# Performance work log

Hardware: AMD Instinct MI355X
Metric: run time of the kernel (lower is better)

The kernel has to match this reference:

```python
import jax, jax.numpy as jnp
import numpy as np

N_HEADS, EMB_DIM, K_DIM, V_DIM = 16, 1024, 64, 64
B, L = 4, 2048


def setup_inputs() -> dict:
    key = jax.random.key(0)
    ks = jax.random.split(key, 7)
    scale = 1.0 / np.sqrt(EMB_DIM)
    return {
        "query": jax.random.normal(ks[0], (B, L, EMB_DIM), dtype=jnp.float32),
        "key": jax.random.normal(ks[1], (B, L, EMB_DIM), dtype=jnp.float32),
        "value": jax.random.normal(ks[2], (B, L, EMB_DIM), dtype=jnp.float32),
        "pad_mask": jnp.ones((B, L), dtype=jnp.int32),
        # Linear weights stored as (in, out); torch Linear computes x @ W.T with W (out, in)
        "Wq": jax.random.normal(ks[3], (EMB_DIM, N_HEADS * K_DIM), dtype=jnp.float32) * scale,
        "Wk": jax.random.normal(ks[4], (EMB_DIM, N_HEADS * K_DIM), dtype=jnp.float32) * scale,
        "Wv": jax.random.normal(ks[5], (EMB_DIM, N_HEADS * V_DIM), dtype=jnp.float32) * scale,
        "Wo": jax.random.normal(ks[6], (N_HEADS * V_DIM, EMB_DIM), dtype=jnp.float32) * scale,
    }


def reference(query, key, value, pad_mask, Wq, Wk, Wv, Wo):
    batch, Lq, _ = query.shape
    Lk = key.shape[1]
    # projections -> [B, L, H, dk/dv]
    q = (query @ Wq).reshape(batch, Lq, N_HEADS, K_DIM)
    k = (key @ Wk).reshape(batch, Lk, N_HEADS, K_DIM)
    v = (value @ Wv).reshape(batch, Lk, N_HEADS, V_DIM)
    # logits: [B, H, Lq, Lk], scaled by 1/sqrt(dk)
    logits = jnp.einsum("bqhd,bkhd->bhqk", q, k) / np.sqrt(K_DIM).astype(np.float32)
    # causal mask: disallow j > i
    causal = jnp.tril(jnp.ones((Lq, Lk), dtype=bool))
    logits = jnp.where(causal[None, None], logits, -jnp.inf)
    # pad mask: positions with pad_mask == 0 are masked out
    keep = (pad_mask != 0)[:, None, None, :]  # [B,1,1,Lk]
    logits = jnp.where(keep, logits, -jnp.inf)
    probs = jax.nn.softmax(logits, axis=-1)
    attn = jnp.einsum("bhqk,bkhd->bqhd", probs, v).reshape(batch, Lq, N_HEADS * V_DIM)
    return attn @ Wo
```

## Files before the change

### kernel.cpp

```cpp
#include <hip/hip_runtime.h>
#include <hip/hip_bf16.h>

typedef short bf16x8 __attribute__((ext_vector_type(8)));
typedef float f32x4 __attribute__((ext_vector_type(4)));

#define EMB 1024
#define NH 16
#define SEQ 2048
#define BATCH 4
#define MROWS (BATCH * SEQ)

static __device__ inline unsigned short f2bf(float f) {
  unsigned u = __float_as_uint(f);
  u += 0x7fffu + ((u >> 16) & 1u);
  return (unsigned short)(u >> 16);
}

static __device__ inline unsigned cvtpk(float lo, float hi) {
  unsigned r;
  asm("v_cvt_pk_bf16_f32 %0, %1, %2" : "=v"(r) : "v"(lo), "v"(hi));
  return r;
}

static __device__ inline void gload16(const void* g, void* l) {
  __builtin_amdgcn_global_load_lds(
      (const __attribute__((address_space(1))) unsigned int*)g,
      (__attribute__((address_space(3))) unsigned int*)l, 16, 0, 0);
}

__global__ __launch_bounds__(256) void wtrans_kernel(
    const float* w0, const float* w1, const float* w2, const float* w3,
    unsigned short* o0, unsigned short* o1, unsigned short* o2, unsigned short* o3) {
  __shared__ float t[32][33];
  int z = blockIdx.z;
  const float* W = z == 0 ? w0 : z == 1 ? w1 : z == 2 ? w2 : w3;
  unsigned short* O = z == 0 ? o0 : z == 1 ? o1 : z == 2 ? o2 : o3;
  float sc = (z == 0) ? 0.18033688011112042f : 1.0f;
  int bx = blockIdx.x * 32;
  int by = blockIdx.y * 32;
  int tx = threadIdx.x, ty = threadIdx.y;
#pragma unroll
  for (int j = 0; j < 4; ++j)
    t[ty + j * 8][tx] = W[(size_t)(bx + ty + j * 8) * EMB + by + tx];
  __syncthreads();
#pragma unroll
  for (int j = 0; j < 4; ++j)
    O[(size_t)(by + ty + j * 8) * EMB + bx + tx] = f2bf(t[tx][ty + j * 8] * sc);
}

template <int IN_F32, int OUT_MODE>
__global__ __launch_bounds__(256) void gemm_kernel(const void* Ap, const unsigned short* Bt, void* Cp) {
  __shared__ __align__(16) unsigned short As[128 * 64];
  __shared__ __align__(16) unsigned short Bs[128 * 64];
  const int K = EMB;
  int tid = threadIdx.x;
  int lane = tid & 63, wave = tid >> 6;
  int q = lane & 15, g = lane >> 4;
  int qx7 = q & 7;
  int wm = (wave >> 1) * 64, wn = (wave & 1) * 64;
  int lin = blockIdx.x + (blockIdx.y << 3);
  int idx = (lin & 7) * 64 + (lin >> 3);
  int tm = (idx >> 3) * 128, tn = (idx & 7) * 128;
  f32x4 acc[4][4] = {};
  for (int kt = 0; kt < K; kt += 64) {
    if (IN_F32) {
      const float* A = (const float*)Ap;
#pragma unroll
      for (int it = 0; it < 4; ++it) {
        int gid = tid + it * 256;
        int row = gid >> 3, cb = gid & 7;
        const float4* s0 = (const float4*)(A + (size_t)(tm + row) * K + kt + cb * 8);
        float4 x = s0[0], y = s0[1];
        uint4 w;
        w.x = cvtpk(x.x, x.y); w.y = cvtpk(x.z, x.w);
        w.z = cvtpk(y.x, y.y); w.w = cvtpk(y.z, y.w);
        *(uint4*)&As[row * 64 + 8 * (cb ^ (row & 7))] = w;
      }
    } else {
      const unsigned short* A = (const unsigned short*)Ap;
#pragma unroll
      for (int it = 0; it < 4; ++it) {
        int gid = tid + it * 256;
        int row = gid >> 3, cb = gid & 7;
        gload16(A + (size_t)(tm + row) * K + kt + 8 * (cb ^ (row & 7)), &As[gid * 8]);
      }
    }
#pragma unroll
    for (int it = 0; it < 4; ++it) {
      int gid = tid + it * 256;
      int row = gid >> 3, cb = gid & 7;
      gload16(Bt + (size_t)(tn + row) * K + kt + 8 * (cb ^ (row & 7)), &Bs[gid * 8]);
    }
    __syncthreads();
#pragma unroll
    for (int s = 0; s < 2; ++s) {
      bf16x8 af[4], bfr[4];
#pragma unroll
      for (int mf = 0; mf < 4; ++mf)
        af[mf] = *(const bf16x8*)&As[(wm + mf * 16 + q) * 64 + 8 * ((4 * s + g) ^ qx7)];
#pragma unroll
      for (int nf = 0; nf < 4; ++nf)
        bfr[nf] = *(const bf16x8*)&Bs[(wn + nf * 16 + q) * 64 + 8 * ((4 * s + g) ^ qx7)];
#pragma unroll
      for (int mf = 0; mf < 4; ++mf)
#pragma unroll
        for (int nf = 0; nf < 4; ++nf)
          acc[mf][nf] = __builtin_amdgcn_mfma_f32_16x16x32_bf16(af[mf], bfr[nf], acc[mf][nf], 0, 0, 0);
    }
    __syncthreads();
  }
  if (OUT_MODE == 0) {
    unsigned short* C = (unsigned short*)Cp;
#pragma unroll
    for (int mf = 0; mf < 4; ++mf)
#pragma unroll
      for (int nf = 0; nf < 4; ++nf)
#pragma unroll
        for (int r = 0; r < 4; ++r) {
          int row = tm + wm + mf * 16 + 4 * g + r;
          int col = tn + wn + nf * 16 + q;
          C[(size_t)row * EMB + col] = f2bf(acc[mf][nf][r]);
        }
  } else if (OUT_MODE == 1) {
    unsigned short* C = (unsigned short*)Cp;
#pragma unroll
    for (int mf = 0; mf < 4; ++mf) {
      int m0 = tm + wm + mf * 16 + 4 * g;
      int b = m0 >> 11, l = m0 & 2047;
#pragma unroll
      for (int nf = 0; nf < 4; ++nf) {
        int n = tn + wn + nf * 16 + q;
        int h = n >> 6, dv = n & 63;
        uint2 w;
        w.x = cvtpk(acc[mf][nf][0], acc[mf][nf][1]);
        w.y = cvtpk(acc[mf][nf][2], acc[mf][nf][3]);
        *(uint2*)&C[(((size_t)b * NH + h) * 64 + dv) * SEQ + l] = w;
      }
    }
  } else {
    float* C = (float*)Cp;
#pragma unroll
    for (int mf = 0; mf < 4; ++mf)
#pragma unroll
      for (int nf = 0; nf < 4; ++nf)
#pragma unroll
        for (int r = 0; r < 4; ++r) {
          int row = tm + wm + mf * 16 + 4 * g + r;
          int col = tn + wn + nf * 16 + q;
          C[(size_t)row * EMB + col] = acc[mf][nf][r];
        }
  }
}

__global__ __launch_bounds__(256) void attn_kernel(
    const unsigned short* Qb, const unsigned short* Kb, const unsigned short* VTb,
    const int* pad, unsigned short* Ob) {
  __shared__ __align__(16) unsigned short Ks[2][64 * 64];
  __shared__ __align__(16) unsigned short Vs[2][64 * 64];
  __shared__ __align__(16) unsigned short Ps[4][16 * 64];
  int tid = threadIdx.x;
  int lane = tid & 63, wave = tid >> 6;
  int q = lane & 15, g = lane >> 4;
  int qx7 = q & 7;
  int lin = blockIdx.x;
  int idx = (lin & 7) * 128 + (lin >> 3);
  int b = idx >> 8, h = (idx >> 4) & 15, px = idx & 15;

  int srow = tid >> 3, scb = tid & 7;
  int ssw = 8 * (scb ^ (srow & 7));
  const unsigned short* Kbase = Kb + (size_t)b * SEQ * EMB + (size_t)srow * EMB + h * 64 + ssw;
  const unsigned short* Vbase = VTb + (((size_t)(b * NH + h)) * 64 + srow) * SEQ + ssw;

#pragma unroll 1
  for (int half = 0; half < 2; ++half) {
    int c = half ? 31 - px : px;
    int qg = c * 64 + wave * 16 + q;
    const unsigned short* Qrow = Qb + ((size_t)(b * SEQ + qg)) * EMB + h * 64;
    bf16x8 qf0 = *(const bf16x8*)(Qrow + 8 * g);
    bf16x8 qf1 = *(const bf16x8*)(Qrow + 32 + 8 * g);
    f32x4 o[4] = {};
    float m_run = -INFINITY, l_run = 0.f;

#pragma unroll
    for (int it = 0; it < 2; ++it) {
      gload16(Kbase + (size_t)(it * 32) * EMB, &Ks[0][(tid + it * 256) * 8]);
      gload16(Vbase + it * 32 * SEQ, &Vs[0][(tid + it * 256) * 8]);
    }
    __syncthreads();

#pragma unroll 1
    for (int t = 0; t <= c; ++t) {
      int kvt = t * 64;
      int cur = t & 1;
      if (t < c) {
#pragma unroll
        for (int it = 0; it < 2; ++it) {
          gload16(Kbase + (size_t)(kvt + 64 + it * 32) * EMB, &Ks[cur ^ 1][(tid + it * 256) * 8]);
          gload16(Vbase + (size_t)(kvt + 64) + it * 32 * SEQ, &Vs[cur ^ 1][(tid + it * 256) * 8]);
        }
      }
      int pv = pad[b * SEQ + kvt + lane];
      unsigned long long pmask = __ballot(pv != 0);
      f32x4 sf[4] = {};
      __builtin_amdgcn_s_setprio(1);
#pragma unroll
      for (int s = 0; s < 2; ++s) {
#pragma unroll
        for (int mf = 0; mf < 4; ++mf) {
          bf16x8 kf = *(const bf16x8*)&Ks[cur][(mf * 16 + q) * 64 + 8 * ((4 * s + g) ^ qx7)];
          sf[mf] = __builtin_amdgcn_mfma_f32_16x16x32_bf16(kf, s ? qf1 : qf0, sf[mf], 0, 0, 0);
        }
      }
      __builtin_amdgcn_s_setprio(0);
      float tmax = -INFINITY;
      bool full = (t < c) && (pmask == ~0ull);
      if (full) {
#pragma unroll
        for (int mf = 0; mf < 4; ++mf)
#pragma unroll
          for (int r = 0; r < 4; ++r) tmax = fmaxf(tmax, sf[mf][r]);
      } else {
#pragma unroll
        for (int mf = 0; mf < 4; ++mf)
#pragma unroll
          for (int r = 0; r < 4; ++r) {
            int kvl = mf * 16 + 4 * g + r;
            bool keep = (kvt + kvl <= qg) && ((pmask >> kvl) & 1ULL);
            float sv = keep ? sf[mf][r] : -INFINITY;
            sf[mf][r] = sv;
            tmax = fmaxf(tmax, sv);
          }
      }
      tmax = fmaxf(tmax, __shfl_xor(tmax, 16));
      tmax = fmaxf(tmax, __shfl_xor(tmax, 32));
      if (!__all(tmax <= m_run + 8.0f)) {
        float m_new = fmaxf(m_run, tmax);
        float alpha = __builtin_amdgcn_exp2f(m_run - m_new);
        l_run *= alpha;
#pragma unroll
        for (int mv = 0; mv < 4; ++mv) o[mv] *= alpha;
        m_run = m_new;
      }
      float rsum = 0.f;
      float pvv[16];
#pragma unroll
      for (int mf = 0; mf < 4; ++mf)
#pragma unroll
        for (int r = 0; r < 4; ++r) {
          float p = __builtin_amdgcn_exp2f(sf[mf][r] - m_run);
          pvv[mf * 4 + r] = p;
          rsum += p;
        }
#pragma unroll
      for (int mf = 0; mf < 4; ++mf) {
        uint2 w;
        w.x = cvtpk(pvv[mf * 4 + 0], pvv[mf * 4 + 1]);
        w.y = cvtpk(pvv[mf * 4 + 2], pvv[mf * 4 + 3]);
        int cbP = 2 * mf + (g >> 1);
        *(uint2*)&Ps[wave][q * 64 + 8 * (cbP ^ qx7) + 4 * (g & 1)] = w;
      }
      rsum += __shfl_xor(rsum, 16);
      rsum += __shfl_xor(rsum, 32);
      l_run += rsum;
      __builtin_amdgcn_s_setprio(1);
#pragma unroll
      for (int s = 0; s < 2; ++s) {
        bf16x8 pb = *(const bf16x8*)&Ps[wave][q * 64 + 8 * ((4 * s + g) ^ qx7)];
#pragma unroll
        for (int mv = 0; mv < 4; ++mv) {
          bf16x8 va = *(const bf16x8*)&Vs[cur][(mv * 16 + q) * 64 + 8 * ((4 * s + g) ^ qx7)];
          o[mv] = __builtin_amdgcn_mfma_f32_16x16x32_bf16(va, pb, o[mv], 0, 0, 0);
        }
      }
      __builtin_amdgcn_s_setprio(0);
      __syncthreads();
    }
    float inv = 1.0f / l_run;
    unsigned short* Orow = Ob + ((size_t)(b * SEQ + qg)) * EMB + h * 64;
#pragma unroll
    for (int mv = 0; mv < 4; ++mv) {
      uint2 w;
      w.x = cvtpk(o[mv][0] * inv, o[mv][1] * inv);
      w.y = cvtpk(o[mv][2] * inv, o[mv][3] * inv);
      *(uint2*)&Orow[mv * 16 + 4 * g] = w;
    }
  }
}

extern "C" void kernel_launch(void* const* d_in, const int* in_sizes, int n_in,
                              void* d_out, int out_size, void* d_ws, size_t ws_size,
                              hipStream_t stream) {
  const float* query = (const float*)d_in[0];
  const float* key   = (const float*)d_in[1];
  const float* value = (const float*)d_in[2];
  const int*   pad   = (const int*)d_in[3];
  const float* Wq = (const float*)d_in[4];
  const float* Wk = (const float*)d_in[5];
  const float* Wv = (const float*)d_in[6];
  const float* Wo = (const float*)d_in[7];

  unsigned short* WqT = (unsigned short*)d_ws;
  unsigned short* WkT = WqT + (size_t)EMB * EMB;
  unsigned short* WvT = WkT + (size_t)EMB * EMB;
  unsigned short* WoT = WvT + (size_t)EMB * EMB;
  unsigned short* Qb  = WoT + (size_t)EMB * EMB;
  unsigned short* Kb  = Qb + (size_t)MROWS * EMB;
  unsigned short* VTb = Kb + (size_t)MROWS * EMB;
  unsigned short* Ab  = VTb + (size_t)MROWS * EMB;

  wtrans_kernel<<<dim3(EMB / 32, EMB / 32, 4), dim3(32, 8), 0, stream>>>(
      Wq, Wk, Wv, Wo, WqT, WkT, WvT, WoT);
  gemm_kernel<1, 0><<<dim3(8, 64), 256, 0, stream>>>(query, WqT, Qb);
  gemm_kernel<1, 0><<<dim3(8, 64), 256, 0, stream>>>(key, WkT, Kb);
  gemm_kernel<1, 1><<<dim3(8, 64), 256, 0, stream>>>(value, WvT, VTb);
  attn_kernel<<<dim3(1024), 256, 0, stream>>>(Qb, Kb, VTb, pad, Ab);
  gemm_kernel<0, 2><<<dim3(8, 64), 256, 0, stream>>>(Ab, WoT, d_out);
}
```

Before: 208.4 us.

## Process both causal query tiles in one KV pass to share K/V loads

The attention kernel used to handle its two paired query tiles (px and 31-px) one after the other, streaming K/V twice. Now both tiles' state is kept in registers and a single KV sweep up to the longer tile's length serves both. The shorter tile's work is predicated off once its causal limit is passed. This removes redundant K/V global/LDS loads and gives each wave more independent MFMA work per tile, at the cost of extra registers and LDS for a second P buffer, which may reduce occupancy.

```diff
diff --git a/kernel.cpp b/kernel.cpp
--- a/kernel.cpp
+++ b/kernel.cpp
@@ -157,7 +157,8 @@
     const int* pad, unsigned short* Ob) {
   __shared__ __align__(16) unsigned short Ks[2][64 * 64];
   __shared__ __align__(16) unsigned short Vs[2][64 * 64];
-  __shared__ __align__(16) unsigned short Ps[4][16 * 64];
+  __shared__ __align__(16) unsigned short PsA[4][16 * 64];
+  __shared__ __align__(16) unsigned short PsB[4][16 * 64];
   int tid = threadIdx.x;
   int lane = tid & 63, wave = tid >> 6;
   int q = lane & 15, g = lane >> 4;
@@ -165,125 +166,195 @@
   int lin = blockIdx.x;
   int idx = (lin & 7) * 128 + (lin >> 3);
   int b = idx >> 8, h = (idx >> 4) & 15, px = idx & 15;
+  int cA = px, cB = 31 - px;
+  int qgA = cA * 64 + wave * 16 + q;
+  int qgB = cB * 64 + wave * 16 + q;
+
+  const unsigned short* QrowA = Qb + ((size_t)(b * SEQ + qgA)) * EMB + h * 64;
+  const unsigned short* QrowB = Qb + ((size_t)(b * SEQ + qgB)) * EMB + h * 64;
+  bf16x8 qfA0 = *(const bf16x8*)(QrowA + 8 * g);
+  bf16x8 qfA1 = *(const bf16x8*)(QrowA + 32 + 8 * g);
+  bf16x8 qfB0 = *(const bf16x8*)(QrowB + 8 * g);
+  bf16x8 qfB1 = *(const bf16x8*)(QrowB + 32 + 8 * g);
+
+  f32x4 oA[4] = {}, oB[4] = {};
+  float mA = -INFINITY, lA = 0.f, mB = -INFINITY, lB = 0.f;
 
   int srow = tid >> 3, scb = tid & 7;
   int ssw = 8 * (scb ^ (srow & 7));
   const unsigned short* Kbase = Kb + (size_t)b * SEQ * EMB + (size_t)srow * EMB + h * 64 + ssw;
   const unsigned short* Vbase = VTb + (((size_t)(b * NH + h)) * 64 + srow) * SEQ + ssw;
 
+#pragma unroll
+  for (int it = 0; it < 2; ++it) {
+    gload16(Kbase + (size_t)(it * 32) * EMB, &Ks[0][(tid + it * 256) * 8]);
+    gload16(Vbase + (size_t)(it * 32) * SEQ, &Vs[0][(tid + it * 256) * 8]);
+  }
+  __syncthreads();
+
 #pragma unroll 1
-  for (int half = 0; half < 2; ++half) {
-    int c = half ? 31 - px : px;
-    int qg = c * 64 + wave * 16 + q;
-    const unsigned short* Qrow = Qb + ((size_t)(b * SEQ + qg)) * EMB + h * 64;
-    bf16x8 qf0 = *(const bf16x8*)(Qrow + 8 * g);
-    bf16x8 qf1 = *(const bf16x8*)(Qrow + 32 + 8 * g);
-    f32x4 o[4] = {};
-    float m_run = -INFINITY, l_run = 0.f;
-
-#pragma unroll
-    for (int it = 0; it < 2; ++it) {
-      gload16(Kbase + (size_t)(it * 32) * EMB, &Ks[0][(tid + it * 256) * 8]);
-      gload16(Vbase + it * 32 * SEQ, &Vs[0][(tid + it * 256) * 8]);
-    }
-    __syncthreads();
-
-#pragma unroll 1
-    for (int t = 0; t <= c; ++t) {
-      int kvt = t * 64;
-      int cur = t & 1;
-      if (t < c) {
-#pragma unroll
-        for (int it = 0; it < 2; ++it) {
-          gload16(Kbase + (size_t)(kvt + 64 + it * 32) * EMB, &Ks[cur ^ 1][(tid + it * 256) * 8]);
-          gload16(Vbase + (size_t)(kvt + 64) + it * 32 * SEQ, &Vs[cur ^ 1][(tid + it * 256) * 8]);
-        }
-      }
-      int pv = pad[b * SEQ + kvt + lane];
-      unsigned long long pmask = __ballot(pv != 0);
-      f32x4 sf[4] = {};
-      __builtin_amdgcn_s_setprio(1);
-#pragma unroll
-      for (int s = 0; s < 2; ++s) {
-#pragma unroll
-        for (int mf = 0; mf < 4; ++mf) {
-          bf16x8 kf = *(const bf16x8*)&Ks[cur][(mf * 16 + q) * 64 + 8 * ((4 * s + g) ^ qx7)];
-          sf[mf] = __builtin_amdgcn_mfma_f32_16x16x32_bf16(kf, s ? qf1 : qf0, sf[mf], 0, 0, 0);
-        }
-      }
-      __builtin_amdgcn_s_setprio(0);
+  for (int t = 0; t <= cB; ++t) {
+    int kvt = t * 64;
+    int cur = t & 1;
+    if (t < cB) {
+#pragma unroll
+      for (int it = 0; it < 2; ++it) {
+        gload16(Kbase + (size_t)(kvt + 64 + it * 32) * EMB, &Ks[cur ^ 1][(tid + it * 256) * 8]);
+        gload16(Vbase + (size_t)(kvt + 64) + (size_t)(it * 32) * SEQ, &Vs[cur ^ 1][(tid + it * 256) * 8]);
+      }
+    }
+    int pv = pad[b * SEQ + kvt + lane];
+    unsigned long long pmask = __ballot(pv != 0);
+    bool doA = (t <= cA);
+
+    f32x4 sfA[4] = {}, sfB[4] = {};
+    __builtin_amdgcn_s_setprio(1);
+#pragma unroll
+    for (int s = 0; s < 2; ++s) {
+#pragma unroll
+      for (int mf = 0; mf < 4; ++mf) {
+        bf16x8 kf = *(const bf16x8*)&Ks[cur][(mf * 16 + q) * 64 + 8 * ((4 * s + g) ^ qx7)];
+        if (doA) sfA[mf] = __builtin_amdgcn_mfma_f32_16x16x32_bf16(kf, s ? qfA1 : qfA0, sfA[mf], 0, 0, 0);
+        sfB[mf] = __builtin_amdgcn_mfma_f32_16x16x32_bf16(kf, s ? qfB1 : qfB0, sfB[mf], 0, 0, 0);
+      }
+    }
+    __builtin_amdgcn_s_setprio(0);
+
+    if (doA) {
       float tmax = -INFINITY;
-      bool full = (t < c) && (pmask == ~0ull);
+      bool full = (t < cA) && (pmask == ~0ull);
       if (full) {
 #pragma unroll
         for (int mf = 0; mf < 4; ++mf)
 #pragma unroll
-          for (int r = 0; r < 4; ++r) tmax = fmaxf(tmax, sf[mf][r]);
+          for (int r = 0; r < 4; ++r) tmax = fmaxf(tmax, sfA[mf][r]);
       } else {
 #pragma unroll
         for (int mf = 0; mf < 4; ++mf)
 #pragma unroll
           for (int r = 0; r < 4; ++r) {
             int kvl = mf * 16 + 4 * g + r;
-            bool keep = (kvt + kvl <= qg) && ((pmask >> kvl) & 1ULL);
-            float sv = keep ? sf[mf][r] : -INFINITY;
-            sf[mf][r] = sv;
+            bool keep = (kvt + kvl <= qgA) && ((pmask >> kvl) & 1ULL);
+            float sv = keep ? sfA[mf][r] : -INFINITY;
+            sfA[mf][r] = sv;
             tmax = fmaxf(tmax, sv);
           }
       }
       tmax = fmaxf(tmax, __shfl_xor(tmax, 16));
       tmax = fmaxf(tmax, __shfl_xor(tmax, 32));
-      if (!__all(tmax <= m_run + 8.0f)) {
-        float m_new = fmaxf(m_run, tmax);
-        float alpha = __builtin_amdgcn_exp2f(m_run - m_new);
-        l_run *= alpha;
-#pragma unroll
-        for (int mv = 0; mv < 4; ++mv) o[mv] *= alpha;
-        m_run = m_new;
+      if (!__all(tmax <= mA + 8.0f)) {
+        float m_new = fmaxf(mA, tmax);
+        float alpha = __builtin_amdgcn_exp2f(mA - m_new);
+        lA *= alpha;
+#pragma unroll
+        for (int mv = 0; mv < 4; ++mv) oA[mv] *= alpha;
+        mA = m_new;
       }
       float rsum = 0.f;
-      float pvv[16];
+      float pv0[16];
 #pragma unroll
       for (int mf = 0; mf < 4; ++mf)
 #pragma unroll
         for (int r = 0; r < 4; ++r) {
-          float p = __builtin_amdgcn_exp2f(sf[mf][r] - m_run);
-          pvv[mf * 4 + r] = p;
+          float p = __builtin_amdgcn_exp2f(sfA[mf][r] - mA);
+          pv0[mf * 4 + r] = p;
           rsum += p;
         }
 #pragma unroll
       for (int mf = 0; mf < 4; ++mf) {
         uint2 w;
-        w.x = cvtpk(pvv[mf * 4 + 0], pvv[mf * 4 + 1]);
-        w.y = cvtpk(pvv[mf * 4 + 2], pvv[mf * 4 + 3]);
+        w.x = cvtpk(pv0[mf * 4 + 0], pv0[mf * 4 + 1]);
+        w.y = cvtpk(pv0[mf * 4 + 2], pv0[mf * 4 + 3]);
         int cbP = 2 * mf + (g >> 1);
-        *(uint2*)&Ps[wave][q * 64 + 8 * (cbP ^ qx7) + 4 * (g & 1)] = w;
+        *(uint2*)&PsA[wave][q * 64 + 8 * (cbP ^ qx7) + 4 * (g & 1)] = w;
       }
       rsum += __shfl_xor(rsum, 16);
       rsum += __shfl_xor(rsum, 32);
-      l_run += rsum;
-      __builtin_amdgcn_s_setprio(1);
-#pragma unroll
-      for (int s = 0; s < 2; ++s) {
-        bf16x8 pb = *(const bf16x8*)&Ps[wave][q * 64 + 8 * ((4 * s + g) ^ qx7)];
-#pragma unroll
-        for (int mv = 0; mv < 4; ++mv) {
-          bf16x8 va = *(const bf16x8*)&Vs[cur][(mv * 16 + q) * 64 + 8 * ((4 * s + g) ^ qx7)];
-          o[mv] = __builtin_amdgcn_mfma_f32_16x16x32_bf16(va, pb, o[mv], 0, 0, 0);
+      lA += rsum;
+    }
+
+    {
+      float tmax = -INFINITY;
+      bool full = (t < cB) && (pmask == ~0ull);
+      if (full) {
+#pragma unroll
+        for (int mf = 0; mf < 4; ++mf)
+#pragma unroll
+          for (int r = 0; r < 4; ++r) tmax = fmaxf(tmax, sfB[mf][r]);
+      } else {
+#pragma unroll
+        for (int mf = 0; mf < 4; ++mf)
+#pragma unroll
+          for (int r = 0; r < 4; ++r) {
+            int kvl = mf * 16 + 4 * g + r;
+            bool keep = (kvt + kvl <= qgB) && ((pmask >> kvl) & 1ULL);
+            float sv = keep ? sfB[mf][r] : -INFINITY;
+            sfB[mf][r] = sv;
+            tmax = fmaxf(tmax, sv);
+          }
+      }
+      tmax = fmaxf(tmax, __shfl_xor(tmax, 16));
+      tmax = fmaxf(tmax, __shfl_xor(tmax, 32));
+      if (!__all(tmax <= mB + 8.0f)) {
+        float m_new = fmaxf(mB, tmax);
+        float alpha = __builtin_amdgcn_exp2f(mB - m_new);
+        lB *= alpha;
+#pragma unroll
+        for (int mv = 0; mv < 4; ++mv) oB[mv] *= alpha;
+        mB = m_new;
+      }
+      float rsum = 0.f;
+      float pv1[16];
+#pragma unroll
+      for (int mf = 0; mf < 4; ++mf)
+#pragma unroll
+        for (int r = 0; r < 4; ++r) {
+          float p = __builtin_amdgcn_exp2f(sfB[mf][r] - mB);
+          pv1[mf * 4 + r] = p;
+          rsum += p;
         }
-      }
-      __builtin_amdgcn_s_setprio(0);
-      __syncthreads();
-    }
-    float inv = 1.0f / l_run;
-    unsigned short* Orow = Ob + ((size_t)(b * SEQ + qg)) * EMB + h * 64;
-#pragma unroll
-    for (int mv = 0; mv < 4; ++mv) {
-      uint2 w;
-      w.x = cvtpk(o[mv][0] * inv, o[mv][1] * inv);
-      w.y = cvtpk(o[mv][2] * inv, o[mv][3] * inv);
-      *(uint2*)&Orow[mv * 16 + 4 * g] = w;
-    }
+#pragma unroll
+      for (int mf = 0; mf < 4; ++mf) {
+        uint2 w;
+        w.x = cvtpk(pv1[mf * 4 + 0], pv1[mf * 4 + 1]);
+        w.y = cvtpk(pv1[mf * 4 + 2], pv1[mf * 4 + 3]);
+        int cbP = 2 * mf + (g >> 1);
+        *(uint2*)&PsB[wave][q * 64 + 8 * (cbP ^ qx7) + 4 * (g & 1)] = w;
+      }
+      rsum += __shfl_xor(rsum, 16);
+      rsum += __shfl_xor(rsum, 32);
+      lB += rsum;
+    }
+
+    __builtin_amdgcn_s_setprio(1);
+#pragma unroll
+    for (int s = 0; s < 2; ++s) {
+      bf16x8 pbA = *(const bf16x8*)&PsA[wave][q * 64 + 8 * ((4 * s + g) ^ qx7)];
+      bf16x8 pbB = *(const bf16x8*)&PsB[wave][q * 64 + 8 * ((4 * s + g) ^ qx7)];
+#pragma unroll
+      for (int mv = 0; mv < 4; ++mv) {
+        bf16x8 va = *(const bf16x8*)&Vs[cur][(mv * 16 + q) * 64 + 8 * ((4 * s + g) ^ qx7)];
+        if (doA) oA[mv] = __builtin_amdgcn_mfma_f32_16x16x32_bf16(va, pbA, oA[mv], 0, 0, 0);
+        oB[mv] = __builtin_amdgcn_mfma_f32_16x16x32_bf16(va, pbB, oB[mv], 0, 0, 0);
+      }
+    }
+    __builtin_amdgcn_s_setprio(0);
+    __syncthreads();
+  }
+
+  float invA = 1.0f / lA;
+  float invB = 1.0f / lB;
+  unsigned short* OrowA = Ob + ((size_t)(b * SEQ + qgA)) * EMB + h * 64;
+  unsigned short* OrowB = Ob + ((size_t)(b * SEQ + qgB)) * EMB + h * 64;
+#pragma unroll
+  for (int mv = 0; mv < 4; ++mv) {
+    uint2 wa, wb;
+    wa.x = cvtpk(oA[mv][0] * invA, oA[mv][1] * invA);
+    wa.y = cvtpk(oA[mv][2] * invA, oA[mv][3] * invA);
+    wb.x = cvtpk(oB[mv][0] * invB, oB[mv][1] * invB);
+    wb.y = cvtpk(oB[mv][2] * invB, oB[mv][3] * invB);
+    *(uint2*)&OrowA[mv * 16 + 4 * g] = wa;
+    *(uint2*)&OrowB[mv * 16 + 4 * g] = wb;
   }
 }
 
```

Result: slower. 243.1 us (+16.7%).
